# Performance work log

Hardware: AMD Instinct MI355X
Metric: run time of the kernel (lower is better)

The kernel has to match this reference:

```python
import jax, jax.numpy as jnp
import numpy as np

N_FEATURES = 512
N_LAYERS = 128
BATCH = 2048
PI = np.pi


def setup_inputs() -> dict:
    key = jax.random.key(0)
    k0, k1, k2, k3, k4 = jax.random.split(key, 5)
    nA = N_FEATURES // 2            # angles per A layer (even pairs)
    nB = (N_FEATURES - 1) // 2      # angles per B layer (odd pairs)
    LB = N_LAYERS // 2
    LA = N_LAYERS - LB              # equal when N_LAYERS even
    return {
        "cmplx": jax.random.normal(k0, (BATCH, N_FEATURES, 2), dtype=jnp.float32),
        "angleA0": jax.random.uniform(k1, (LA, nA), jnp.float32, -PI, PI),
        "angleA1": jax.random.uniform(k2, (LA, nA), jnp.float32, -PI, PI),
        "angleB0": jax.random.uniform(k3, (LB, nB), jnp.float32, -PI, PI),
        "angleB1": jax.random.uniform(k4, (LB, nB), jnp.float32, -PI, PI),
        "omega": jnp.zeros((N_FEATURES,), jnp.float32),
    }


def _mzi(a, b, ang0, ang1):
    # MZI = DC . PS(ang1) . DC . PS(ang0) acting on mode pair (a, b)
    # U = 1/2 [[e^{i phi}(e^{i th}-1),    i(e^{i th}+1)   ],
    #          [i e^{i phi}(e^{i th}+1),  (1 - e^{i th})  ]]
    ephi = jnp.exp(1j * ang0)
    eth = jnp.exp(1j * ang1)
    t = 0.5 * (eth - 1.0)
    u = 0.5 * (eth + 1.0)
    na = ephi * t * a + 1j * u * b
    nb = 1j * ephi * u * a - t * b
    return na, nb


def _layer_A(x, a0, a1):
    # pairs (0,1),(2,3),...
    a = x[:, 0::2]
    b = x[:, 1::2]
    na, nb = _mzi(a, b, a0, a1)
    return jnp.stack([na, nb], axis=-1).reshape(x.shape)


def _layer_B(x, b0, b1):
    # pairs (1,2),(3,4),...; endpoints 0 and N-1 pass through (N even)
    N = x.shape[1]
    a = x[:, 1:N - 1:2]
    b = x[:, 2:N:2]
    na, nb = _mzi(a, b, b0, b1)
    mid = jnp.stack([na, nb], axis=-1).reshape(x.shape[0], N - 2)
    return jnp.concatenate([x[:, :1], mid, x[:, -1:]], axis=1)


def reference(cmplx, angleA0, angleA1, angleB0, angleB1, omega):
    x = cmplx[..., 0] + 1j * cmplx[..., 1]   # [B, N] complex64

    def step(x, angs):
        a0, a1, b0, b1 = angs
        x = _layer_A(x, a0, a1)
        x = _layer_B(x, b0, b1)
        return x, None

    x, _ = jax.lax.scan(step, x, (angleA0, angleA1, angleB0, angleB1))
    out = x * jnp.exp(1j * omega)            # complex diagonal phase
    return jnp.stack([out.real, out.imag], axis=-1)
```

## Files before the change

### kernel.cpp

```cpp
#include <hip/hip_runtime.h>

#define NF 512
#define MB 2048
#define CSTRIDE 256
#define PL (NF * NF)
#define LDT 72

typedef __attribute__((ext_vector_type(8))) short bf16x8;
typedef __attribute__((ext_vector_type(4))) float f32x4;
typedef __attribute__((ext_vector_type(4))) int i32x4;

__device__ __forceinline__ float2 cmul(float2 a, float2 b) {
  return make_float2(fmaf(a.x, b.x, -(a.y * b.y)), fmaf(a.x, b.y, a.y * b.x));
}
__device__ __forceinline__ float2 cfma(float2 a, float2 b, float2 c) {
  return make_float2(fmaf(a.x, b.x, fmaf(-a.y, b.y, c.x)),
                     fmaf(a.x, b.y, fmaf(a.y, b.x, c.y)));
}
__device__ __forceinline__ unsigned short f2bf(float f) {
  union { float f; unsigned u; } v; v.f = f;
  unsigned r = v.u + 0x7FFF + ((v.u >> 16) & 1);
  return (unsigned short)(r >> 16);
}

__global__ __launch_bounds__(256) void prep_kernel(
    const float* __restrict__ a0, const float* __restrict__ a1,
    const float* __restrict__ b0, const float* __restrict__ b1,
    float4* __restrict__ cA, float4* __restrict__ cB)
{
  const int l = blockIdx.x, tid = threadIdx.x;
  {
    float ang0 = a0[l * 256 + tid], ang1 = a1[l * 256 + tid];
    float se, ce, st, ct;
    sincosf(ang0, &se, &ce);
    sincosf(ang1, &st, &ct);
    float2 ephi = make_float2(ce, se);
    float2 tt = make_float2(0.5f * (ct - 1.0f), 0.5f * st);
    float2 uu = make_float2(0.5f * (ct + 1.0f), 0.5f * st);
    float2 C1 = cmul(ephi, tt);
    float2 C2 = make_float2(-uu.y, uu.x);
    float2 eu = cmul(ephi, uu);
    float2 C3 = make_float2(-eu.y, eu.x);
    float2 C4 = make_float2(-tt.x, -tt.y);
    float4* dst = cA + (size_t)(l * CSTRIDE + tid) * 2;
    dst[0] = make_float4(C1.x, C1.y, C2.x, C2.y);
    dst[1] = make_float4(C3.x, C3.y, C4.x, C4.y);
  }
  if (tid < 255) {
    float ang0 = b0[l * 255 + tid], ang1 = b1[l * 255 + tid];
    float se, ce, st, ct;
    sincosf(ang0, &se, &ce);
    sincosf(ang1, &st, &ct);
    float2 ephi = make_float2(ce, se);
    float2 tt = make_float2(0.5f * (ct - 1.0f), 0.5f * st);
    float2 uu = make_float2(0.5f * (ct + 1.0f), 0.5f * st);
    float2 C1 = cmul(ephi, tt);
    float2 C2 = make_float2(-uu.y, uu.x);
    float2 eu = cmul(ephi, uu);
    float2 C3 = make_float2(-eu.y, eu.x);
    float2 C4 = make_float2(-tt.x, -tt.y);
    float4* dst = cB + (size_t)(l * CSTRIDE + tid) * 2;
    dst[0] = make_float4(C1.x, C1.y, C2.x, C2.y);
    dst[1] = make_float4(C3.x, C3.y, C4.x, C4.y);
  } else {
    float4* dst = cB + (size_t)(l * CSTRIDE + 255) * 2;
    dst[0] = make_float4(0.f, 0.f, 0.f, 0.f);
    dst[1] = make_float4(0.f, 0.f, 0.f, 0.f);
  }
}

struct MZS { float2 a0, b0, a1, b1; };

__device__ __forceinline__ void mzi_apply(const float4& k0, const float4& k1,
                                          float2& a, float2& b) {
  float2 c1 = make_float2(k0.x, k0.y), c2 = make_float2(k0.z, k0.w);
  float2 c3 = make_float2(k1.x, k1.y), c4 = make_float2(k1.z, k1.w);
  float2 na = cfma(c2, b, cmul(c1, a));
  float2 nb = cfma(c4, b, cmul(c3, a));
  a = na; b = nb;
}
__device__ __forceinline__ float2 mzi_bnd(const float4& k0, const float4& k1,
                                          float2& a, float2 b, bool en) {
  float2 d1 = make_float2(k0.x, k0.y), d2 = make_float2(k0.z, k0.w);
  float2 d3 = make_float2(k1.x, k1.y), d4 = make_float2(k1.z, k1.w);
  float2 na = cfma(d2, b, cmul(d1, a));
  float2 nb = cfma(d4, b, cmul(d3, a));
  if (en) a = na;
  return en ? nb : make_float2(0.f, 0.f);
}
__device__ __forceinline__ void load_bank(float4 (&K)[8],
    const float4* __restrict__ cA, const float4* __restrict__ cB, int l, int q0)
{
  const float4* pa = cA + (size_t)l * (CSTRIDE * 2) + (size_t)q0 * 2;
  const float4* pb = cB + (size_t)l * (CSTRIDE * 2) + (size_t)q0 * 2;
  K[0] = pa[0]; K[1] = pa[1]; K[2] = pa[2]; K[3] = pa[3];
  K[4] = pb[0]; K[5] = pb[1]; K[6] = pb[2]; K[7] = pb[3];
}
__device__ __forceinline__ void step_state(const float4 (&K)[8], int L, bool hasBnd,
                                           MZS& s)
{
  mzi_apply(K[0], K[1], s.a0, s.b0);
  mzi_apply(K[2], K[3], s.a1, s.b1);
  float xnx = __shfl_down(s.a0.x, 1);
  float xny = __shfl_down(s.a0.y, 1);
  float2 xn = (L == 63) ? make_float2(0.f, 0.f) : make_float2(xnx, xny);
  float2 nbo = mzi_bnd(K[6], K[7], s.b1, xn, hasBnd);
  mzi_apply(K[4], K[5], s.b0, s.a1);
  float px = __shfl_up(nbo.x, 1);
  float py = __shfl_up(nbo.y, 1);
  if (L > 0) s.a0 = make_float2(px, py);
}

__global__ __launch_bounds__(64) void chunk_mesh(
    const float4* __restrict__ cA, const float4* __restrict__ cB,
    unsigned short* __restrict__ Cb)
{
  const int bid = blockIdx.x;
  const int m = bid >> 9;
  const int cb = bid & 511;
  const int j = (cb & 7) * 64 + (cb >> 3);
  const int L = threadIdx.x;
  const int p0 = j >> 1;
  int ws = p0 - 63; ws = ws < 0 ? 0 : (ws > 128 ? 128 : ws);
  const int q0 = ws + 2 * L, q1 = q0 + 1;
  const bool hasBnd = (q1 < 255);

  MZS s;
  s.a0 = make_float2((2 * q0     == j) ? 1.f : 0.f, 0.f);
  s.b0 = make_float2((2 * q0 + 1 == j) ? 1.f : 0.f, 0.f);
  s.a1 = make_float2((2 * q1     == j) ? 1.f : 0.f, 0.f);
  s.b1 = make_float2((2 * q1 + 1 == j) ? 1.f : 0.f, 0.f);

  const int l0 = m * 16;
  float4 K0[8], K1[8];
  load_bank(K0, cA, cB, l0 + 0, q0);
  load_bank(K1, cA, cB, l0 + 1, q0);
#pragma unroll 1
  for (int i = 0; i < 14; i += 2) {
    step_state(K0, L, hasBnd, s);
    load_bank(K0, cA, cB, l0 + ((i + 2 < 16) ? i + 2 : 15), q0);
    step_state(K1, L, hasBnd, s);
    load_bank(K1, cA, cB, l0 + ((i + 3 < 16) ? i + 3 : 15), q0);
  }
  step_state(K0, L, hasBnd, s);
  step_state(K1, L, hasBnd, s);

  unsigned short* Cr = Cb + (size_t)m * 2 * PL;
  unsigned short* Ci = Cr + PL;
  if ((m & 1) == 0) {
    const int col0 = 2 * q0;
    ushort4 vr, vi;
    vr.x = f2bf(s.a0.x); vr.y = f2bf(s.b0.x); vr.z = f2bf(s.a1.x); vr.w = f2bf(s.b1.x);
    vi.x = f2bf(s.a0.y); vi.y = f2bf(s.b0.y); vi.z = f2bf(s.a1.y); vi.w = f2bf(s.b1.y);
    *(ushort4*)&Cr[(size_t)j * NF + col0] = vr;
    *(ushort4*)&Ci[(size_t)j * NF + col0] = vi;
    const int z0 = (col0 + 256) & 511;
    const int z1 = (col0 + 258) & 511;
    const ushort2 zz = make_ushort2(0, 0);
    *(ushort2*)&Cr[(size_t)j * NF + z0] = zz;
    *(ushort2*)&Cr[(size_t)j * NF + z1] = zz;
    *(ushort2*)&Ci[(size_t)j * NF + z0] = zz;
    *(ushort2*)&Ci[(size_t)j * NF + z1] = zz;
  } else {
    const int rows[4] = {2 * q0, 2 * q0 + 1, 2 * q1, 2 * q1 + 1};
    const float2 vals[4] = {s.a0, s.b0, s.a1, s.b1};
#pragma unroll
    for (int e = 0; e < 4; ++e) {
      Cr[(size_t)rows[e] * NF + j] = f2bf(vals[e].x);
      Ci[(size_t)rows[e] * NF + j] = f2bf(vals[e].y);
    }
#pragma unroll
    for (int e = 0; e < 4; ++e) {
      const int row = (2 * ws + 256 + 4 * L + e) & 511;
      Cr[(size_t)row * NF + j] = 0;
      Ci[(size_t)row * NF + j] = 0;
    }
  }
}

__device__ void prod_tile(
    const unsigned short* __restrict__ Agr, const unsigned short* __restrict__ Agi,
    const unsigned short* __restrict__ Bgr, const unsigned short* __restrict__ Bgi,
    unsigned short* __restrict__ Or, unsigned short* __restrict__ Oi,
    int bm, int bn, int klo, int khi, int tid,
    unsigned short (*Ars)[LDT], unsigned short (*Ais)[LDT],
    unsigned short (*Brs)[LDT], unsigned short (*Bis)[LDT])
{
  const int w = tid >> 6, wm = w & 1, wn = w >> 1, lane = tid & 63;
  f32x4 acc_r[2], acc_i[2];
#pragma unroll
  for (int nf = 0; nf < 2; ++nf) {
    acc_r[nf] = (f32x4){0.f, 0.f, 0.f, 0.f};
    acc_i[nf] = (f32x4){0.f, 0.f, 0.f, 0.f};
  }
  const int sar = tid >> 3, sak = (tid & 7) * 8;
  const int sbr = tid >> 2, sbk = (tid & 3) * 16;

  for (int k0 = klo; k0 < khi; k0 += 64) {
    const uint4* gar = (const uint4*)(Agr + (size_t)(bm + sar) * NF + k0 + sak);
    const uint4* gai = (const uint4*)(Agi + (size_t)(bm + sar) * NF + k0 + sak);
    const uint4* gbr = (const uint4*)(Bgr + (size_t)(bn + sbr) * NF + k0 + sbk);
    const uint4* gbi = (const uint4*)(Bgi + (size_t)(bn + sbr) * NF + k0 + sbk);
    uint4 ar = gar[0];
    uint4 ai = gai[0];
    uint4 br0 = gbr[0], br1 = gbr[1];
    uint4 bi0 = gbi[0], bi1 = gbi[1];

    __syncthreads();

    *(uint4*)&Ars[sar][sak]     = ar;
    *(uint4*)&Ais[sar][sak]     = ai;
    *(uint4*)&Brs[sbr][sbk]     = br0;
    *(uint4*)&Brs[sbr][sbk + 8] = br1;
    *(uint4*)&Bis[sbr][sbk]     = bi0;
    *(uint4*)&Bis[sbr][sbk + 8] = bi1;

    __syncthreads();

#pragma unroll
    for (int kk = 0; kk < 2; ++kk) {
      const int ko = kk * 32 + (lane >> 4) * 8;
      bf16x8 afr = *(const bf16x8*)&Ars[wm * 16 + (lane & 15)][ko];
      bf16x8 afi = *(const bf16x8*)&Ais[wm * 16 + (lane & 15)][ko];
      i32x4 neg = (i32x4)afi ^ (int)0x80008000;
      bf16x8 afin = (bf16x8)neg;
#pragma unroll
      for (int nf = 0; nf < 2; ++nf) {
        bf16x8 bfr = *(const bf16x8*)&Brs[wn * 32 + nf * 16 + (lane & 15)][ko];
        bf16x8 bfi = *(const bf16x8*)&Bis[wn * 32 + nf * 16 + (lane & 15)][ko];
        acc_r[nf] = __builtin_amdgcn_mfma_f32_16x16x32_bf16(afr,  bfr, acc_r[nf], 0, 0, 0);
        acc_r[nf] = __builtin_amdgcn_mfma_f32_16x16x32_bf16(afin, bfi, acc_r[nf], 0, 0, 0);
        acc_i[nf] = __builtin_amdgcn_mfma_f32_16x16x32_bf16(afr,  bfi, acc_i[nf], 0, 0, 0);
        acc_i[nf] = __builtin_amdgcn_mfma_f32_16x16x32_bf16(afi,  bfr, acc_i[nf], 0, 0, 0);
      }
    }
  }

  const int dn0 = bn + wn * 32 + (lane & 15);
  const int dm0 = bm + wm * 16 + (lane >> 4) * 4;
#pragma unroll
  for (int nf = 0; nf < 2; ++nf) {
    const int n = dn0 + nf * 16;
#pragma unroll
    for (int r = 0; r < 4; ++r) {
      Or[(size_t)(dm0 + r) * NF + n] = f2bf(acc_r[nf][r]);
      Oi[(size_t)(dm0 + r) * NF + n] = f2bf(acc_i[nf][r]);
    }
  }
}

__global__ __launch_bounds__(256) void prodW_kernel(
    const unsigned short* __restrict__ Cb, unsigned short* __restrict__ Wp)
{
  __shared__ __align__(16) unsigned short Ars[32][LDT];
  __shared__ __align__(16) unsigned short Ais[32][LDT];
  __shared__ __align__(16) unsigned short Brs[64][LDT];
  __shared__ __align__(16) unsigned short Bis[64][LDT];

  const int tid = threadIdx.x;
  const int z = blockIdx.x >> 7;
  const int t = blockIdx.x & 127;
  const int bm = (t >> 3) * 32, bn = (t & 7) * 64;
  const unsigned short* CT = Cb + (size_t)(2 * z) * 2 * PL;
  const unsigned short* CN = Cb + (size_t)(2 * z + 1) * 2 * PL;
  unsigned short* O = Wp + (size_t)z * 2 * PL;
  const int hw = 35;
  const unsigned short* A; const unsigned short* B;
  if (z == 0) { A = CT; B = CN; }
  else        { A = CN; B = CT; }
  int klo = bm - hw; { int u = bn - hw; if (u > klo) klo = u; }
  if (klo < 0) klo = 0; klo &= ~63;
  int khi = bm + 32 + hw; { int u = bn + 64 + hw; if (u < khi) khi = u; }
  if (khi > NF) khi = NF; khi = (khi + 63) & ~63;
  prod_tile(A, A + PL, B, B + PL, O, O + PL, bm, bn, klo, khi, tid,
            Ars, Ais, Brs, Bis);
}

__global__ __launch_bounds__(256) void prodU_kernel(
    const unsigned short* __restrict__ Wp, unsigned short* __restrict__ Up)
{
  __shared__ __align__(16) unsigned short Ars[32][LDT];
  __shared__ __align__(16) unsigned short Ais[32][LDT];
  __shared__ __align__(16) unsigned short Brs[64][LDT];
  __shared__ __align__(16) unsigned short Bis[64][LDT];

  const int tid = threadIdx.x;
  const int t = blockIdx.x;
  const int bm = (t >> 3) * 32, bn = (t & 7) * 64;
  const unsigned short* W0T = Wp;
  const unsigned short* W1N = Wp + (size_t)2 * PL;
  const int hw = 70;
  int klo = bm - hw; { int u = bn - hw; if (u > klo) klo = u; }
  if (klo < 0) klo = 0; klo &= ~63;
  int khi = bm + 32 + hw; { int u = bn + 64 + hw; if (u < khi) khi = u; }
  if (khi > NF) khi = NF; khi = (khi + 63) & ~63;
  prod_tile(W1N, W1N + PL, W0T, W0T + PL, Up, Up + PL, bm, bn, klo, khi, tid,
            Ars, Ais, Brs, Bis);
}

__global__ __launch_bounds__(256) void gemm_kernel(
    const float2* __restrict__ Xf,
    const unsigned short* __restrict__ Ur, const unsigned short* __restrict__ Ui,
    const float* __restrict__ omega, float2* __restrict__ Y)
{
  __shared__ __align__(16) unsigned short Ars[32][LDT];
  __shared__ __align__(16) unsigned short Ais[32][LDT];
  __shared__ __align__(16) unsigned short Brs[64][LDT];
  __shared__ __align__(16) unsigned short Bis[64][LDT];

  const int tid = threadIdx.x;
  const int w = tid >> 6, wm = w & 1, wn = w >> 1;
  const int lane = tid & 63;
  const int bm = (blockIdx.x >> 3) * 32;
  const int bn = (blockIdx.x & 7) * 64;

  int klo = bn - 140; if (klo < 0) klo = 0; klo &= ~63;
  int khi = bn + 204; if (khi > NF) khi = NF; khi = (khi + 63) & ~63;

  f32x4 acc_r[2], acc_i[2];
#pragma unroll
  for (int nf = 0; nf < 2; ++nf) {
    acc_r[nf] = (f32x4){0.f, 0.f, 0.f, 0.f};
    acc_i[nf] = (f32x4){0.f, 0.f, 0.f, 0.f};
  }
  const int sar = tid >> 3, sak = (tid & 7) * 8;
  const int sbr = tid >> 2, sbk = (tid & 3) * 16;

  for (int k0 = klo; k0 < khi; k0 += 64) {
    ushort4 ar2[2], ai2[2];
    const float4* xs = (const float4*)(Xf + (size_t)(bm + sar) * NF + k0 + sak);
#pragma unroll
    for (int h = 0; h < 2; ++h) {
      float4 v0 = xs[2 * h], v1 = xs[2 * h + 1];
      ar2[h].x = f2bf(v0.x); ai2[h].x = f2bf(v0.y);
      ar2[h].y = f2bf(v0.z); ai2[h].y = f2bf(v0.w);
      ar2[h].z = f2bf(v1.x); ai2[h].z = f2bf(v1.y);
      ar2[h].w = f2bf(v1.z); ai2[h].w = f2bf(v1.w);
    }
    const uint4* gbr = (const uint4*)(Ur + (size_t)(bn + sbr) * NF + k0 + sbk);
    const uint4* gbi = (const uint4*)(Ui + (size_t)(bn + sbr) * NF + k0 + sbk);
    uint4 br0 = gbr[0], br1 = gbr[1];
    uint4 bi0 = gbi[0], bi1 = gbi[1];

    if (k0 > klo) __syncthreads();

    *(ushort4*)&Ars[sar][sak]     = ar2[0];
    *(ushort4*)&Ars[sar][sak + 4] = ar2[1];
    *(ushort4*)&Ais[sar][sak]     = ai2[0];
    *(ushort4*)&Ais[sar][sak + 4] = ai2[1];
    *(uint4*)&Brs[sbr][sbk]       = br0;
    *(uint4*)&Brs[sbr][sbk + 8]   = br1;
    *(uint4*)&Bis[sbr][sbk]       = bi0;
    *(uint4*)&Bis[sbr][sbk + 8]   = bi1;

    __syncthreads();

#pragma unroll
    for (int kk = 0; kk < 2; ++kk) {
      const int ko = kk * 32 + (lane >> 4) * 8;
      bf16x8 afr = *(const bf16x8*)&Ars[wm * 16 + (lane & 15)][ko];
      bf16x8 afi = *(const bf16x8*)&Ais[wm * 16 + (lane & 15)][ko];
      i32x4 neg = (i32x4)afi ^ (int)0x80008000;
      bf16x8 afin = (bf16x8)neg;
#pragma unroll
      for (int nf = 0; nf < 2; ++nf) {
        bf16x8 bfr = *(const bf16x8*)&Brs[wn * 32 + nf * 16 + (lane & 15)][ko];
        bf16x8 bfi = *(const bf16x8*)&Bis[wn * 32 + nf * 16 + (lane & 15)][ko];
        acc_r[nf] = __builtin_amdgcn_mfma_f32_16x16x32_bf16(afr,  bfr, acc_r[nf], 0, 0, 0);
        acc_r[nf] = __builtin_amdgcn_mfma_f32_16x16x32_bf16(afin, bfi, acc_r[nf], 0, 0, 0);
        acc_i[nf] = __builtin_amdgcn_mfma_f32_16x16x32_bf16(afr,  bfi, acc_i[nf], 0, 0, 0);
        acc_i[nf] = __builtin_amdgcn_mfma_f32_16x16x32_bf16(afi,  bfr, acc_i[nf], 0, 0, 0);
      }
    }
  }

  const int dn0 = bn + wn * 32 + (lane & 15);
  const int dm0 = bm + wm * 16 + (lane >> 4) * 4;
#pragma unroll
  for (int nf = 0; nf < 2; ++nf) {
    const int n = dn0 + nf * 16;
    float sn, cn;
    sincosf(omega[n], &sn, &cn);
#pragma unroll
    for (int r = 0; r < 4; ++r) {
      float yr = acc_r[nf][r], yi = acc_i[nf][r];
      Y[(size_t)(dm0 + r) * NF + n] =
          make_float2(fmaf(yr, cn, -(yi * sn)), fmaf(yr, sn, yi * cn));
    }
  }
}

extern "C" void kernel_launch(void* const* d_in, const int* in_sizes, int n_in,
                              void* d_out, int out_size, void* d_ws, size_t ws_size,
                              hipStream_t stream) {
  const float2* Xf   = (const float2*)d_in[0];
  const float* a0    = (const float*)d_in[1];
  const float* a1    = (const float*)d_in[2];
  const float* b0    = (const float*)d_in[3];
  const float* b1    = (const float*)d_in[4];
  const float* omega = (const float*)d_in[5];

  size_t off = 0;
  float4* cA = (float4*)((char*)d_ws + off); off += (size_t)64 * CSTRIDE * 2 * sizeof(float4);
  float4* cB = (float4*)((char*)d_ws + off); off += (size_t)64 * CSTRIDE * 2 * sizeof(float4);
  unsigned short* Cb = (unsigned short*)((char*)d_ws + off); off += (size_t)4 * 2 * PL * 2;
  unsigned short* Wp = (unsigned short*)((char*)d_ws + off); off += (size_t)2 * 2 * PL * 2;
  unsigned short* Up = (unsigned short*)((char*)d_ws + off); off += (size_t)1 * 2 * PL * 2;
  float2* Y = (float2*)d_out;

  prep_kernel<<<64, 256, 0, stream>>>(a0, a1, b0, b1, cA, cB);
  chunk_mesh<<<2048, 64, 0, stream>>>(cA, cB, Cb);
  prodW_kernel<<<256, 256, 0, stream>>>(Cb, Wp);
  prodU_kernel<<<128, 256, 0, stream>>>(Wp, Up);
  gemm_kernel<<<(MB / 32) * (NF / 64), 256, 0, stream>>>(Xf, Up, Up + PL, omega, Y);
}
```

Baseline: 52.62 us.

## Build two 32-layer chunk matrices and drop the intermediate product kernel

Each chunk_mesh block now propagates 32 layers instead of 16, with triple-buffered coefficient loads, so only two chunk transfer matrices are produced. The prodW stage is removed and prodU multiplies the two chunk matrices directly. This saves one kernel launch and one banded complex GEMM pass plus its workspace traffic. In exchange, the serial mesh stage doubles its per-block work while launching half as many blocks, which can lengthen that stage's latency.

```diff
diff --git a/kernel.cpp b/kernel.cpp
--- a/kernel.cpp
+++ b/kernel.cpp
@@ -131,23 +131,27 @@
   s.a1 = make_float2((2 * q1     == j) ? 1.f : 0.f, 0.f);
   s.b1 = make_float2((2 * q1 + 1 == j) ? 1.f : 0.f, 0.f);
 
-  const int l0 = m * 16;
-  float4 K0[8], K1[8];
+  const int l0 = m * 32;
+  float4 K0[8], K1[8], K2[8];
   load_bank(K0, cA, cB, l0 + 0, q0);
   load_bank(K1, cA, cB, l0 + 1, q0);
+  load_bank(K2, cA, cB, l0 + 2, q0);
+
 #pragma unroll 1
-  for (int i = 0; i < 14; i += 2) {
+  for (int i = 0; i < 30; i += 3) {
     step_state(K0, L, hasBnd, s);
-    load_bank(K0, cA, cB, l0 + ((i + 2 < 16) ? i + 2 : 15), q0);
+    load_bank(K0, cA, cB, l0 + ((i + 3 < 32) ? i + 3 : 31), q0);
     step_state(K1, L, hasBnd, s);
-    load_bank(K1, cA, cB, l0 + ((i + 3 < 16) ? i + 3 : 15), q0);
+    load_bank(K1, cA, cB, l0 + ((i + 4 < 32) ? i + 4 : 31), q0);
+    step_state(K2, L, hasBnd, s);
+    load_bank(K2, cA, cB, l0 + ((i + 5 < 32) ? i + 5 : 31), q0);
   }
   step_state(K0, L, hasBnd, s);
   step_state(K1, L, hasBnd, s);
 
   unsigned short* Cr = Cb + (size_t)m * 2 * PL;
   unsigned short* Ci = Cr + PL;
-  if ((m & 1) == 0) {
+  if (m == 0) {
     const int col0 = 2 * q0;
     ushort4 vr, vi;
     vr.x = f2bf(s.a0.x); vr.y = f2bf(s.b0.x); vr.z = f2bf(s.a1.x); vr.w = f2bf(s.b1.x);
@@ -249,8 +253,8 @@
   }
 }
 
-__global__ __launch_bounds__(256) void prodW_kernel(
-    const unsigned short* __restrict__ Cb, unsigned short* __restrict__ Wp)
+__global__ __launch_bounds__(256) void prodU_kernel(
+    const unsigned short* __restrict__ Cb, unsigned short* __restrict__ Up)
 {
   __shared__ __align__(16) unsigned short Ars[32][LDT];
   __shared__ __align__(16) unsigned short Ais[32][LDT];
@@ -258,43 +262,16 @@
   __shared__ __align__(16) unsigned short Bis[64][LDT];
 
   const int tid = threadIdx.x;
-  const int z = blockIdx.x >> 7;
-  const int t = blockIdx.x & 127;
-  const int bm = (t >> 3) * 32, bn = (t & 7) * 64;
-  const unsigned short* CT = Cb + (size_t)(2 * z) * 2 * PL;
-  const unsigned short* CN = Cb + (size_t)(2 * z + 1) * 2 * PL;
-  unsigned short* O = Wp + (size_t)z * 2 * PL;
-  const int hw = 35;
-  const unsigned short* A; const unsigned short* B;
-  if (z == 0) { A = CT; B = CN; }
-  else        { A = CN; B = CT; }
-  int klo = bm - hw; { int u = bn - hw; if (u > klo) klo = u; }
-  if (klo < 0) klo = 0; klo &= ~63;
-  int khi = bm + 32 + hw; { int u = bn + 64 + hw; if (u < khi) khi = u; }
-  if (khi > NF) khi = NF; khi = (khi + 63) & ~63;
-  prod_tile(A, A + PL, B, B + PL, O, O + PL, bm, bn, klo, khi, tid,
-            Ars, Ais, Brs, Bis);
-}
-
-__global__ __launch_bounds__(256) void prodU_kernel(
-    const unsigned short* __restrict__ Wp, unsigned short* __restrict__ Up)
-{
-  __shared__ __align__(16) unsigned short Ars[32][LDT];
-  __shared__ __align__(16) unsigned short Ais[32][LDT];
-  __shared__ __align__(16) unsigned short Brs[64][LDT];
-  __shared__ __align__(16) unsigned short Bis[64][LDT];
-
-  const int tid = threadIdx.x;
   const int t = blockIdx.x;
   const int bm = (t >> 3) * 32, bn = (t & 7) * 64;
-  const unsigned short* W0T = Wp;
-  const unsigned short* W1N = Wp + (size_t)2 * PL;
+  const unsigned short* C0T = Cb;
+  const unsigned short* C1N = Cb + (size_t)2 * PL;
   const int hw = 70;
   int klo = bm - hw; { int u = bn - hw; if (u > klo) klo = u; }
   if (klo < 0) klo = 0; klo &= ~63;
   int khi = bm + 32 + hw; { int u = bn + 64 + hw; if (u < khi) khi = u; }
   if (khi > NF) khi = NF; khi = (khi + 63) & ~63;
-  prod_tile(W1N, W1N + PL, W0T, W0T + PL, Up, Up + PL, bm, bn, klo, khi, tid,
+  prod_tile(C1N, C1N + PL, C0T, C0T + PL, Up, Up + PL, bm, bn, klo, khi, tid,
             Ars, Ais, Brs, Bis);
 }
 
@@ -403,14 +380,12 @@
   size_t off = 0;
   float4* cA = (float4*)((char*)d_ws + off); off += (size_t)64 * CSTRIDE * 2 * sizeof(float4);
   float4* cB = (float4*)((char*)d_ws + off); off += (size_t)64 * CSTRIDE * 2 * sizeof(float4);
-  unsigned short* Cb = (unsigned short*)((char*)d_ws + off); off += (size_t)4 * 2 * PL * 2;
-  unsigned short* Wp = (unsigned short*)((char*)d_ws + off); off += (size_t)2 * 2 * PL * 2;
+  unsigned short* Cb = (unsigned short*)((char*)d_ws + off); off += (size_t)2 * 2 * PL * 2;
   unsigned short* Up = (unsigned short*)((char*)d_ws + off); off += (size_t)1 * 2 * PL * 2;
   float2* Y = (float2*)d_out;
 
   prep_kernel<<<64, 256, 0, stream>>>(a0, a1, b0, b1, cA, cB);
-  chunk_mesh<<<2048, 64, 0, stream>>>(cA, cB, Cb);
-  prodW_kernel<<<256, 256, 0, stream>>>(Cb, Wp);
-  prodU_kernel<<<128, 256, 0, stream>>>(Wp, Up);
+  chunk_mesh<<<1024, 64, 0, stream>>>(cA, cB, Cb);
+  prodU_kernel<<<128, 256, 0, stream>>>(Cb, Up);
   gemm_kernel<<<(MB / 32) * (NF / 64), 256, 0, stream>>>(Xf, Up, Up + PL, omega, Y);
 }
```

New measurement: 46.12 us. 12.4% less time.
